# Performance work log

Hardware: AMD Instinct MI355X
Metric: run time of the kernel (lower is better)

The kernel has to match this reference:

```python
import jax, jax.numpy as jnp
import numpy as np

# tinygemm asymmetric int4 convention
QUANT_MIN, QUANT_MAX = 0, 15
MID_POINT = (QUANT_MAX + QUANT_MIN + 1) / 2.0  # 8.0
OUT_F, IN_F, GROUP = 8192, 8192, 128
M_TOKENS = 64


def setup_inputs() -> dict:
    key = jax.random.key(0)
    kx, kw = jax.random.split(key)
    x = jax.random.normal(kx, (M_TOKENS, IN_F), dtype=jnp.float32)
    # Materialize quantized params exactly as quantize_weight_tinygemm does.
    w = jax.random.normal(kw, (OUT_F, IN_F), dtype=jnp.float32) * 0.02
    ng = IN_F // GROUP
    wg = w.reshape(OUT_F, ng, GROUP)
    min_val = wg.min(axis=2)
    max_val = wg.max(axis=2)
    scale = jnp.maximum((max_val - min_val) / float(QUANT_MAX - QUANT_MIN), 1.1920929e-7)
    zero_point = min_val + scale * MID_POINT
    min_val_recon = zero_point - scale * MID_POINT
    q = jnp.clip(jnp.round((wg - min_val_recon[..., None]) / scale[..., None]),
                 QUANT_MIN, QUANT_MAX).astype(jnp.int32)
    int_data = q.reshape(OUT_F, IN_F)  # values in [0, 15]
    # tinygemm layout: (n_groups, out_features, 2) with [..., 0]=scale, [..., 1]=zero_point
    scale_and_zero = jnp.stack([scale, zero_point], axis=-1).transpose(1, 0, 2)
    return {"x": x, "int_data": int_data, "scale_and_zero": scale_and_zero}


def reference(x, int_data, scale_and_zero):
    # Dequant: w = (q - MID_POINT) * scale + zero_point, per group of GROUP along in_features.
    ng = IN_F // GROUP
    q = int_data.reshape(OUT_F, ng, GROUP).astype(x.dtype)
    scale = scale_and_zero[..., 0].T[:, :, None]       # (OUT_F, ng, 1)
    zero_point = scale_and_zero[..., 1].T[:, :, None]  # (OUT_F, ng, 1)
    w = ((q - MID_POINT) * scale + zero_point).reshape(OUT_F, IN_F)
    return x @ w.T  # (M, OUT_F)
```

## Files before the change

kernel.cpp:

```cpp
#include <hip/hip_runtime.h>
#include <hip/hip_bf16.h>


#define OUT_F 8192
#define IN_F  8192
#define M_TOK 64
#define GROUP 128
#define BN    64
#define KSPLIT 4
#define KR    (IN_F / KSPLIT)
#define GROUPS (KR / GROUP)

typedef short short8 __attribute__((ext_vector_type(8)));
typedef float f32x4  __attribute__((ext_vector_type(4)));
typedef int   int4v  __attribute__((ext_vector_type(4)));

__device__ __forceinline__ unsigned pk(float lo, float hi) {
    __hip_bfloat162 h = __float22bfloat162_rn(float2{lo, hi});
    unsigned r;
    __builtin_memcpy(&r, &h, sizeof(r));
    return r;
}

__global__ void zero_out(float* __restrict__ p) {
    const int i = (blockIdx.x * 256 + threadIdx.x) * 4;
    *(float4*)(p + i) = float4{0.f, 0.f, 0.f, 0.f};
}

__global__ __launch_bounds__(512, 4)
void woq_gemm(const float* __restrict__ x,
              const int*   __restrict__ qw,
              const float* __restrict__ sz,
              float*       __restrict__ outp) {
    __shared__ int lds_x[2][4096];
    __shared__ int lds_w[2][4096];

    const int t    = threadIdx.x;
    const int lane = t & 63;
    const int wv   = t >> 6;
    const int wn   = wv & 3;
    const int kh   = wv >> 2;
    const int n0   = blockIdx.x * BN;
    const int k0   = blockIdx.y * KR;

    const int nlo  = lane & 15;
    const int quad = lane >> 4;
    const int row  = wn * 16 + nlo;
    const int n1   = n0 + row;

    const int tr = t >> 5;
    const int kc = t & 31;

    f32x4 acc[4];
#pragma unroll
    for (int mi = 0; mi < 4; ++mi) acc[mi] = (f32x4){0.f, 0.f, 0.f, 0.f};

    int4v  wq[4];
    float2 sc[4];
    float4 xs[4];

    auto stage_load = [&](int g) {
        const int kg = k0 + g * GROUP;
#pragma unroll
        for (int i = 0; i < 4; ++i) {
            const int r = i * 16 + tr;
            wq[i] = __builtin_nontemporal_load(
                (const int4v*)(qw + (size_t)(n0 + r) * IN_F + kg + kc * 4));
        }
        const int gg = kg >> 7;
#pragma unroll
        for (int i = 0; i < 4; ++i) {
            const int r = i * 16 + tr;
            sc[i] = *(const float2*)(sz + ((size_t)gg * OUT_F + n0 + r) * 2);
        }
#pragma unroll
        for (int j = 0; j < 2; ++j) {
            const int slot  = t + 512 * j;
            const int chunk = slot >> 6;
            const int l     = slot & 63;
            const int m     = ((chunk & 3) << 4) + (l & 15);
            const int kk    = ((chunk >> 2) << 5) + ((l >> 4) << 3);
            const float4* p = (const float4*)(x + (size_t)m * IN_F + kg + kk);
            xs[2 * j]     = p[0];
            xs[2 * j + 1] = p[1];
        }
    };

    auto stage_write = [&](int buf) {
        int* wb = lds_w[buf];
#pragma unroll
        for (int i = 0; i < 4; ++i) {
            const int r = i * 16 + tr;
            const float s = sc[i].x;
            const float c = fmaf(-8.f, sc[i].x, sc[i].y);
            int2 v;
            v.x = (int)pk(fmaf((float)wq[i].x, s, c), fmaf((float)wq[i].y, s, c));
            v.y = (int)pk(fmaf((float)wq[i].z, s, c), fmaf((float)wq[i].w, s, c));
            const int idx = (r * 64 + kc * 2) ^ ((r & 7) << 2);
            *(int2*)&wb[idx] = v;
        }
        int* xb = lds_x[buf];
#pragma unroll
        for (int j = 0; j < 2; ++j) {
            const int slot = t + 512 * j;
            int4v bv;
            bv.x = (int)pk(xs[2 * j].x,     xs[2 * j].y);
            bv.y = (int)pk(xs[2 * j].z,     xs[2 * j].w);
            bv.z = (int)pk(xs[2 * j + 1].x, xs[2 * j + 1].y);
            bv.w = (int)pk(xs[2 * j + 1].z, xs[2 * j + 1].w);
            *(int4v*)&xb[slot * 4] = bv;
        }
    };

    stage_load(0);
    stage_write(0);
    __syncthreads();

    for (int g = 0; g < GROUPS; ++g) {
        if (g + 1 < GROUPS) stage_load(g + 1);

        const int* xb = lds_x[g & 1];
        const int* wb = lds_w[g & 1];
#pragma unroll
        for (int s = 0; s < 2; ++s) {
            const int ks = kh * 2 + s;
            const int bidx = (row * 64 + ks * 16 + quad * 4) ^ ((row & 7) << 2);
            const short8 b = *(const short8*)&wb[bidx];
            short8 a[4];
#pragma unroll
            for (int mi = 0; mi < 4; ++mi)
                a[mi] = *(const short8*)&xb[((ks * 4 + mi) * 64 + lane) * 4];
#pragma unroll
            for (int mi = 0; mi < 4; ++mi)
                acc[mi] = __builtin_amdgcn_mfma_f32_16x16x32_bf16(a[mi], b, acc[mi], 0, 0, 0);
        }

        if (g + 1 < GROUPS) {
            stage_write((g + 1) & 1);
            __syncthreads();
        }
    }

    __syncthreads();
    f32x4* redp = (f32x4*)&lds_x[0][0];
    if (kh == 1) {
#pragma unroll
        for (int mi = 0; mi < 4; ++mi)
            redp[(wn * 4 + mi) * 64 + lane] = acc[mi];
    }
    __syncthreads();
    if (kh == 0) {
#pragma unroll
        for (int mi = 0; mi < 4; ++mi)
            acc[mi] += redp[(wn * 4 + mi) * 64 + lane];
#pragma unroll
        for (int mi = 0; mi < 4; ++mi)
#pragma unroll
            for (int r = 0; r < 4; ++r)
                atomicAdd(outp + (size_t)(mi * 16 + quad * 4 + r) * OUT_F + n1, acc[mi][r]);
    }
}

extern "C" void kernel_launch(void* const* d_in, const int* in_sizes, int n_in,
                              void* d_out, int out_size, void* d_ws, size_t ws_size,
                              hipStream_t stream) {
    const float* x  = (const float*)d_in[0];
    const int*   qw = (const int*)d_in[1];
    const float* sz = (const float*)d_in[2];
    float* out = (float*)d_out;

    zero_out<<<dim3((M_TOK * OUT_F) / (256 * 4)), 256, 0, stream>>>(out);
    woq_gemm<<<dim3(OUT_F / BN, KSPLIT), 512, 0, stream>>>(x, qw, sz, out);
}
```

Baseline: 366.8 us.

## Prefetch weight tiles two groups ahead and use a lightweight LDS barrier

Restructures the main loop so that quantized weight loads are issued two K-groups ahead into alternating register sets, while x and scales stay one group ahead. The loop is manually unrolled by two, ping-ponging between LDS buffers. __syncthreads is replaced by an inline s_waitcnt lgkmcnt(0) + s_barrier that does not wait on outstanding global loads. The aim is to hide global memory latency on the memory-bound weight stream, at the cost of more registers (an extra int4v[4] set), which could reduce occupancy under launch_bounds(512,4).

```diff
diff --git a/kernel.cpp b/kernel.cpp
--- a/kernel.cpp
+++ b/kernel.cpp
@@ -14,6 +14,8 @@
 typedef short short8 __attribute__((ext_vector_type(8)));
 typedef float f32x4  __attribute__((ext_vector_type(4)));
 typedef int   int4v  __attribute__((ext_vector_type(4)));
+
+#define BAR() asm volatile("s_waitcnt lgkmcnt(0)\n\ts_barrier" ::: "memory")
 
 __device__ __forceinline__ unsigned pk(float lo, float hi) {
     __hip_bfloat162 h = __float22bfloat162_rn(float2{lo, hi});
@@ -55,24 +57,12 @@
 #pragma unroll
     for (int mi = 0; mi < 4; ++mi) acc[mi] = (f32x4){0.f, 0.f, 0.f, 0.f};
 
-    int4v  wq[4];
+    int4v  wqA[4], wqB[4];
+    float4 xs[4];
     float2 sc[4];
-    float4 xs[4];
 
-    auto stage_load = [&](int g) {
+    auto issue_x = [&](int g) {
         const int kg = k0 + g * GROUP;
-#pragma unroll
-        for (int i = 0; i < 4; ++i) {
-            const int r = i * 16 + tr;
-            wq[i] = __builtin_nontemporal_load(
-                (const int4v*)(qw + (size_t)(n0 + r) * IN_F + kg + kc * 4));
-        }
-        const int gg = kg >> 7;
-#pragma unroll
-        for (int i = 0; i < 4; ++i) {
-            const int r = i * 16 + tr;
-            sc[i] = *(const float2*)(sz + ((size_t)gg * OUT_F + n0 + r) * 2);
-        }
 #pragma unroll
         for (int j = 0; j < 2; ++j) {
             const int slot  = t + 512 * j;
@@ -85,8 +75,20 @@
             xs[2 * j + 1] = p[1];
         }
     };
-
-    auto stage_write = [&](int buf) {
+    auto issue_s = [&](int g) {
+        const int gg = (k0 + g * GROUP) >> 7;
+#pragma unroll
+        for (int i = 0; i < 4; ++i)
+            sc[i] = *(const float2*)(sz + ((size_t)gg * OUT_F + n0 + i * 16 + tr) * 2);
+    };
+    auto issue_w = [&](int g, int4v (&wq)[4]) {
+        const int kg = k0 + g * GROUP;
+#pragma unroll
+        for (int i = 0; i < 4; ++i)
+            wq[i] = __builtin_nontemporal_load(
+                (const int4v*)(qw + (size_t)(n0 + i * 16 + tr) * IN_F + kg + kc * 4));
+    };
+    auto write_st = [&](int buf, const int4v (&wq)[4]) {
         int* wb = lds_w[buf];
 #pragma unroll
         for (int i = 0; i < 4; ++i) {
@@ -111,16 +113,7 @@
             *(int4v*)&xb[slot * 4] = bv;
         }
     };
-
-    stage_load(0);
-    stage_write(0);
-    __syncthreads();
-
-    for (int g = 0; g < GROUPS; ++g) {
-        if (g + 1 < GROUPS) stage_load(g + 1);
-
-        const int* xb = lds_x[g & 1];
-        const int* wb = lds_w[g & 1];
+    auto compute = [&](const int* xb, const int* wb) {
 #pragma unroll
         for (int s = 0; s < 2; ++s) {
             const int ks = kh * 2 + s;
@@ -134,10 +127,32 @@
             for (int mi = 0; mi < 4; ++mi)
                 acc[mi] = __builtin_amdgcn_mfma_f32_16x16x32_bf16(a[mi], b, acc[mi], 0, 0, 0);
         }
+    };
 
-        if (g + 1 < GROUPS) {
-            stage_write((g + 1) & 1);
-            __syncthreads();
+    issue_x(0); issue_s(0);
+    issue_w(0, wqA);
+    issue_w(1, wqB);
+    write_st(0, wqA);
+    BAR();
+
+#pragma unroll 1
+    for (int k2 = 0; k2 < GROUPS / 2; ++k2) {
+        const int g = 2 * k2;
+
+        issue_x(g + 1); issue_s(g + 1);
+        if (k2 < GROUPS / 2 - 1) issue_w(g + 2, wqA);
+        compute(lds_x[0], lds_w[0]);
+        write_st(1, wqB);
+        BAR();
+
+        if (k2 < GROUPS / 2 - 1) {
+            issue_x(g + 2); issue_s(g + 2);
+            issue_w(g + 3, wqB);
+            compute(lds_x[1], lds_w[1]);
+            write_st(0, wqA);
+            BAR();
+        } else {
+            compute(lds_x[1], lds_w[1]);
         }
     }
 
```

Result: slower. 414.3 us (+13.0%).
